# Kernel tuning notes

Hardware: AMD Instinct MI355X
Metric: run time of the kernel (lower is better)

## Reference

```python
import jax, jax.numpy as jnp
import numpy as np

NEG_SLOPE = 0.2  # PyG GATv2Conv default negative_slope


def gatv2_conv(x, src, dst, Wl, Wr, att, bias, concat):
    # x: [N, Fin]; src/dst: [E]; Wl/Wr: [Fin, H*C]; att: [H, C]
    N = x.shape[0]
    H, C = att.shape
    xl = (x @ Wl).reshape(N, H, C)
    xr = (x @ Wr).reshape(N, H, C)
    m = jax.nn.leaky_relu(xl[src] + xr[dst], NEG_SLOPE)          # [E,H,C]
    logits = jnp.einsum('ehc,hc->eh', m, att)                    # [E,H]
    lmax = jax.ops.segment_max(logits, dst, num_segments=N)      # stable softmax per dst segment
    ex = jnp.exp(logits - lmax[dst])
    denom = jax.ops.segment_sum(ex, dst, num_segments=N)
    alpha = ex / (denom[dst] + 1e-16)
    out = jax.ops.segment_sum(xl[src] * alpha[:, :, None], dst, num_segments=N)  # [N,H,C]
    out = out.reshape(N, H * C) if concat else out.mean(axis=1)
    return out + bias


def setup_inputs() -> dict:
    key = jax.random.key(0)
    ks = jax.random.split(key, 9)
    bsz, T, n_nodes = 8, 100, 2048
    Cin, hid, H, Cout = 128, 64, 4, 128
    inp = jax.random.normal(ks[0], (bsz, T, n_nodes), jnp.float32)
    ei = jax.random.randint(ks[1], (2, 32768), 0, n_nodes, jnp.int32)
    # remove self loops (PyG remove_self_loops before adding them back)
    ei = ei.at[1].set(jnp.where(ei[0] == ei[1], (ei[1] + 1) % n_nodes, ei[1]))

    def lin(k, fi, fo):
        return jax.random.normal(k, (fi, fo), jnp.float32) / np.sqrt(fi).astype(np.float32)

    return {
        'input': inp, 'edge_index': ei,
        'W_temb': lin(ks[2], T, Cin), 'b_temb': jnp.zeros((Cin,), jnp.float32),
        'Wl1': lin(ks[3], Cin, H * hid), 'Wr1': lin(ks[4], Cin, H * hid),
        'att1': jax.random.normal(ks[5], (H, hid), jnp.float32) / np.sqrt(hid).astype(np.float32),
        'b1': jnp.zeros((H * hid,), jnp.float32),
        'Wl2': lin(ks[6], H * hid, Cout), 'Wr2': lin(ks[7], H * hid, Cout),
        'att2': jax.random.normal(ks[8], (1, Cout), jnp.float32) / np.sqrt(Cout).astype(np.float32),
        'b2': jnp.zeros((Cout,), jnp.float32),
    }


def reference(input, edge_index, W_temb, b_temb, Wl1, Wr1, att1, b1, Wl2, Wr2, att2, b2):
    bsz, T, n_nodes = input.shape
    N = bsz * n_nodes
    # temporal embedding: [B,T,n] -> [B,n,T] @ [T,Cin] -> flatten to [N,Cin]
    x = (jnp.swapaxes(input, 1, 2) @ W_temb + b_temb).reshape(N, -1)
    # faithful to source: edge_index.repeat(1, bsz) tiles edges with NO batch offset;
    # GATv2Conv then adds self loops over all N nodes
    loops = jnp.arange(N, dtype=edge_index.dtype)
    src = jnp.concatenate([jnp.tile(edge_index[0], bsz), loops])
    dst = jnp.concatenate([jnp.tile(edge_index[1], bsz), loops])
    x = gatv2_conv(x, src, dst, Wl1, Wr1, att1, b1, True)
    x = jax.nn.elu(x)
    x = gatv2_conv(x, src, dst, Wl2, Wr2, att2, b2, False)
    return x.reshape(bsz, n_nodes, -1).mean(axis=1)  # [bsz, out_channels]
```

## Files before the change

kernel.cpp:

```cpp
#include <hip/hip_runtime.h>
#include <hip/hip_bf16.h>
#include <math.h>

#define NEG_SLOPE 0.2f

constexpr int BSZ = 8, T = 100, NN = 2048, N = BSZ * NN;
constexpr int CIN = 128, F1 = 256, F2 = 128;
constexpr int E = 32768;
constexpr int KP = 40;
constexpr int MAXDEG = 64;

typedef _Float16 f16x8 __attribute__((ext_vector_type(8)));
typedef float f32x4 __attribute__((ext_vector_type(4)));

__device__ inline float lrelu(float m) { return m > 0.f ? m : NEG_SLOPE * m; }
__device__ inline float eluf(float v) { return v > 0.f ? v : expm1f(v); }

__global__ __launch_bounds__(256) void k_prep(const float* __restrict__ Wt,
        const float* __restrict__ Wl1, const float* __restrict__ Wr1,
        const float* __restrict__ Wl2, const float* __restrict__ Wr2,
        const float* __restrict__ b2,
        _Float16* __restrict__ Tt, _Float16* __restrict__ T1l,
        _Float16* __restrict__ T1r, _Float16* __restrict__ T2l,
        _Float16* __restrict__ T2r, int* __restrict__ cnt, float* __restrict__ out) {
    __shared__ _Float16 tile[32][33];
    const int job = blockIdx.x;
    const int t = threadIdx.x;
    if (job == 144) {
        for (int i = t; i < NN; i += 256) cnt[i] = 0;
        for (int i = t; i < BSZ * F2; i += 256) out[i] = b2[i & (F2 - 1)];
        return;
    }
    int which, base;
    if (job < 16)       { which = 0; base = 0; }
    else if (job < 48)  { which = 1; base = 16; }
    else if (job < 80)  { which = 2; base = 48; }
    else if (job < 112) { which = 3; base = 80; }
    else                { which = 4; base = 112; }
    const int Ks[5] = {100, 128, 128, 256, 256};
    const int Kd[5] = {128, 128, 128, 256, 256};
    const int Nc[5] = {128, 256, 256, 128, 128};
    const float* Wsrc[5] = {Wt, Wl1, Wr1, Wl2, Wr2};
    _Float16* Wdst[5] = {Tt, T1l, T1r, T2l, T2r};
    int rel = job - base;
    int ks = Ks[which], kd = Kd[which], nc = Nc[which];
    int tilesN = nc / 32;
    int tk = (rel / tilesN) * 32, tn = (rel % tilesN) * 32;
    const float* src = Wsrc[which];
    _Float16* dst = Wdst[which];
    int tx = t & 31, ty = t >> 5;
    for (int r = ty; r < 32; r += 8)
        tile[r][tx] = (tk + r < ks) ? (_Float16)src[(tk + r) * nc + tn + tx] : (_Float16)0.f;
    __syncthreads();
    for (int r = ty; r < 32; r += 8)
        dst[(tn + r) * kd + tk + tx] = tile[tx][r];
}

__global__ __launch_bounds__(512) void k_gm1(const float* __restrict__ in,
        const _Float16* __restrict__ Tt, const float* __restrict__ bt,
        const _Float16* __restrict__ T1l, const _Float16* __restrict__ T1r,
        const float* __restrict__ b1, const _Float16* __restrict__ T2l,
        const int* __restrict__ ei, int* __restrict__ cnt, int* __restrict__ srcs,
        float* __restrict__ xl1, float* __restrict__ xr1,
        _Float16* __restrict__ h1h, float* __restrict__ out) {
    const int t = threadIdx.x;
    if (blockIdx.x >= 512) {
        int i = (blockIdx.x - 512) * 512 + t;
        int d = ei[E + i];
        int slot = atomicAdd(&cnt[d], 1);
        if (slot < MAXDEG) srcs[d * MAXDEG + slot] = ei[i];
        return;
    }
    __shared__ __align__(16) char smem[8704 + 43520];
    _Float16* xt = (_Float16*)smem;
    char* sh = smem + 8704;
    const int wave = t >> 6, lane = t & 63;
    const int quad = lane >> 4, l15 = lane & 15;
    const int mat = wave >> 2, cg4 = wave & 3;
    const int row0 = blockIdx.x * 32;
    _Float16* stgT = (_Float16*)sh;
    _Float16* inA  = (_Float16*)(sh + 34816);
    #pragma unroll
    for (int it = 0; it < 4; ++it) {
        int idx = t + it * 512;
        int col = idx >> 4, j = idx & 15;
        *(f16x8*)&stgT[col * 136 + j * 8] = *(const f16x8*)&Tt[col * 128 + j * 8];
    }
    {
        const int b = row0 >> 11, node0 = row0 & (NN - 1);
        const float* ip = in + (size_t)b * T * NN + node0;
        #pragma unroll
        for (int it = 0; it < 8; ++it) {
            int idx = t + it * 512;
            int tt = idx >> 5, n = idx & 31;
            inA[n * 136 + tt] = (tt < T) ? (_Float16)ip[tt * NN + n] : (_Float16)0.f;
        }
    }
    __syncthreads();
    {
        const int wcol = wave * 16 + l15;
        f32x4 a0 = {0,0,0,0}, a1 = {0,0,0,0};
        #pragma unroll
        for (int kt = 0; kt < 128; kt += 32) {
            f16x8 af0 = *(const f16x8*)&inA[l15 * 136 + kt + quad * 8];
            f16x8 af1 = *(const f16x8*)&inA[(16 + l15) * 136 + kt + quad * 8];
            f16x8 bf  = *(const f16x8*)&stgT[wcol * 136 + kt + quad * 8];
            a0 = __builtin_amdgcn_mfma_f32_16x16x32_f16(af0, bf, a0, 0, 0, 0);
            a1 = __builtin_amdgcn_mfma_f32_16x16x32_f16(af1, bf, a1, 0, 0, 0);
        }
        float bv = bt[wcol];
        #pragma unroll
        for (int r = 0; r < 4; ++r) {
            xt[(quad * 4 + r) * 136 + wcol]      = (_Float16)(a0[r] + bv);
            xt[(16 + quad * 4 + r) * 136 + wcol] = (_Float16)(a1[r] + bv);
        }
    }
    __syncthreads();
    _Float16* stg = (_Float16*)sh;
    const int nmats = (row0 < NN) ? 2 : 1;
    f32x4 acc[2][4];
    #pragma unroll
    for (int s = 0; s < 2; ++s)
        #pragma unroll
        for (int c = 0; c < 4; ++c) acc[s][c] = (f32x4){0,0,0,0};
    for (int kt = 0; kt < CIN; kt += 32) {
        if (kt) __syncthreads();
        for (int it = 0; it < nmats * 2; ++it) {
            int idx = t + it * 512;
            int m = idx >> 10, rem = idx & 1023;
            int col = rem >> 2, j = rem & 3;
            const _Float16* src = (m ? T1r : T1l) + col * CIN + kt + j * 8;
            *(f16x8*)&stg[(m * 256 + col) * KP + j * 8] = *(const f16x8*)src;
        }
        __syncthreads();
        f16x8 af0 = *(const f16x8*)&xt[l15 * 136 + kt + quad * 8];
        f16x8 af1 = *(const f16x8*)&xt[(16 + l15) * 136 + kt + quad * 8];
        if (mat < nmats) {
            #pragma unroll
            for (int ct = 0; ct < 4; ++ct) {
                int col = cg4 * 64 + ct * 16 + l15;
                f16x8 bf = *(const f16x8*)&stg[(mat * 256 + col) * KP + quad * 8];
                acc[0][ct] = __builtin_amdgcn_mfma_f32_16x16x32_f16(af0, bf, acc[0][ct], 0, 0, 0);
                acc[1][ct] = __builtin_amdgcn_mfma_f32_16x16x32_f16(af1, bf, acc[1][ct], 0, 0, 0);
            }
        }
    }
    if (row0 < NN) {
        float* dst = mat ? xr1 : xl1;
        #pragma unroll
        for (int s = 0; s < 2; ++s)
            #pragma unroll
            for (int ct = 0; ct < 4; ++ct) {
                int col = cg4 * 64 + ct * 16 + l15;
                #pragma unroll
                for (int r = 0; r < 4; ++r)
                    dst[(row0 + s * 16 + quad * 4 + r) * F1 + col] = acc[s][ct][r];
            }
        return;
    }
    __syncthreads();
    _Float16* stg2 = (_Float16*)sh;
    _Float16* hrow = (_Float16*)(sh + 10240);
    if (mat == 0) {
        #pragma unroll
        for (int ct = 0; ct < 4; ++ct) {
            int col = cg4 * 64 + ct * 16 + l15;
            float bv = b1[col];
            #pragma unroll
            for (int s = 0; s < 2; ++s)
                #pragma unroll
                for (int r = 0; r < 4; ++r)
                    hrow[(s * 16 + quad * 4 + r) * 264 + col] =
                        (_Float16)eluf(acc[s][ct][r] + bv);
        }
    }
    __syncthreads();
    f32x4 c0 = {0,0,0,0}, c1 = {0,0,0,0};
    const int colw = wave * 16 + l15;
    for (int kt = 0; kt < F1; kt += 32) {
        if (kt) __syncthreads();
        {
            int col = t >> 2, j = t & 3;
            *(f16x8*)&stg2[col * KP + j * 8] = *(const f16x8*)&T2l[col * F1 + kt + j * 8];
        }
        __syncthreads();
        f16x8 a0 = *(const f16x8*)&hrow[l15 * 264 + kt + quad * 8];
        f16x8 a1 = *(const f16x8*)&hrow[(16 + l15) * 264 + kt + quad * 8];
        f16x8 bf = *(const f16x8*)&stg2[colw * KP + quad * 8];
        c0 = __builtin_amdgcn_mfma_f32_16x16x32_f16(a0, bf, c0, 0, 0, 0);
        c1 = __builtin_amdgcn_mfma_f32_16x16x32_f16(a1, bf, c1, 0, 0, 0);
    }
    float s8 = c0[0] + c0[1] + c0[2] + c0[3] + c1[0] + c1[1] + c1[2] + c1[3];
    s8 += __shfl_xor(s8, 16, 64);
    s8 += __shfl_xor(s8, 32, 64);
    if (quad == 0)
        atomicAdd(&out[(row0 >> 11) * F2 + colw], s8 * (1.0f / NN));
}

__global__ __launch_bounds__(256) void k_gat1(const int* __restrict__ cnt,
        const int* __restrict__ srcs, const float* __restrict__ xl1,
        const float* __restrict__ xr1, const float* __restrict__ att1,
        const float* __restrict__ b1, _Float16* __restrict__ h1h) {
    __shared__ float lacc[4][F1];
    __shared__ float ldn[4][4];
    const int t = threadIdx.x;
    const int wv = t >> 6, c = t & 63;
    const int d = blockIdx.x;
    int deg = cnt[d]; deg = deg < MAXDEG ? deg : MAXDEG;
    float b[4], at[4], sh[4], acc[4] = {0,0,0,0}, dnl[4] = {0,0,0,0};
    #pragma unroll
    for (int k = 0; k < 4; ++k) {
        b[k]  = xr1[d * F1 + c + 64 * k];
        at[k] = att1[c + 64 * k];
        sh[k] = lrelu(xl1[d * F1 + c + 64 * k] + b[k]) * at[k];
    }
    #pragma unroll
    for (int o = 32; o; o >>= 1) {
        #pragma unroll
        for (int k = 0; k < 4; ++k) sh[k] += __shfl_xor(sh[k], o, 64);
    }
    for (int e = wv; e < deg; e += 4) {
        int s = srcs[d * MAXDEG + e];
        float a[4], p[4];
        #pragma unroll
        for (int k = 0; k < 4; ++k) {
            a[k] = xl1[s * F1 + c + 64 * k];
            p[k] = lrelu(a[k] + b[k]) * at[k];
        }
        #pragma unroll
        for (int o = 32; o; o >>= 1) {
            #pragma unroll
            for (int k = 0; k < 4; ++k) p[k] += __shfl_xor(p[k], o, 64);
        }
        #pragma unroll
        for (int k = 0; k < 4; ++k) {
            float w = 8.0f * __expf(p[k] - sh[k]);
            dnl[k] += w;
            acc[k] = fmaf(w, a[k], acc[k]);
        }
    }
    #pragma unroll
    for (int k = 0; k < 4; ++k) lacc[wv][c + 64 * k] = acc[k];
    if (c < 4) ldn[wv][c] = dnl[c];
    __syncthreads();
    int f = t, h = t >> 6;
    float tot = xl1[d * F1 + f] + lacc[0][f] + lacc[1][f] + lacc[2][f] + lacc[3][f];
    float dnf = 1.0f + ldn[0][h] + ldn[1][h] + ldn[2][h] + ldn[3][h];
    h1h[(size_t)d * F1 + f] = (_Float16)eluf(tot / (dnf + 1e-16f) + b1[f]);
}

__global__ __launch_bounds__(512) void k_gm2loc(const _Float16* __restrict__ h1h,
        const _Float16* __restrict__ T2l, const _Float16* __restrict__ T2r,
        float* __restrict__ xl2, float* __restrict__ xr2) {
    __shared__ __align__(16) _Float16 bs[2 * 128 * KP];
    const int t = threadIdx.x;
    const int wave = t >> 6, lane = t & 63;
    const int quad = lane >> 4, l15 = lane & 15;
    const int mat = wave >> 2, cg4 = wave & 3;
    const int row0 = blockIdx.x * 32;
    f32x4 acc[2][2];
    #pragma unroll
    for (int s = 0; s < 2; ++s)
        #pragma unroll
        for (int c = 0; c < 2; ++c) acc[s][c] = (f32x4){0,0,0,0};
    for (int kt = 0; kt < F1; kt += 32) {
        if (kt) __syncthreads();
        #pragma unroll
        for (int it = 0; it < 2; ++it) {
            int idx = t + it * 512;
            int m = idx >> 9, rem = idx & 511;
            int col = rem >> 2, j = rem & 3;
            const _Float16* src = (m ? T2r : T2l) + col * F1 + kt + j * 8;
            *(f16x8*)&bs[(m * 128 + col) * KP + j * 8] = *(const f16x8*)src;
        }
        __syncthreads();
        f16x8 af0 = *(const f16x8*)&h1h[(size_t)(row0 + l15) * F1 + kt + quad * 8];
        f16x8 af1 = *(const f16x8*)&h1h[(size_t)(row0 + 16 + l15) * F1 + kt + quad * 8];
        #pragma unroll
        for (int ct = 0; ct < 2; ++ct) {
            int col = cg4 * 32 + ct * 16 + l15;
            f16x8 bf = *(const f16x8*)&bs[(mat * 128 + col) * KP + quad * 8];
            acc[0][ct] = __builtin_amdgcn_mfma_f32_16x16x32_f16(af0, bf, acc[0][ct], 0, 0, 0);
            acc[1][ct] = __builtin_amdgcn_mfma_f32_16x16x32_f16(af1, bf, acc[1][ct], 0, 0, 0);
        }
    }
    float* dst = mat ? xr2 : xl2;
    #pragma unroll
    for (int s = 0; s < 2; ++s)
        #pragma unroll
        for (int ct = 0; ct < 2; ++ct) {
            int col = cg4 * 32 + ct * 16 + l15;
            #pragma unroll
            for (int r = 0; r < 4; ++r)
                dst[(row0 + s * 16 + quad * 4 + r) * F2 + col] = acc[s][ct][r];
        }
}

__global__ __launch_bounds__(256) void k_gat2(const int* __restrict__ cnt,
        const int* __restrict__ srcs, const float* __restrict__ xl2,
        const float* __restrict__ xr2, const float* __restrict__ att2,
        float* __restrict__ acc2) {
    const int d = blockIdx.x;
    const int t = threadIdx.x;
    const int wv = t >> 6, c = t & 63;
    int deg = cnt[d]; deg = deg < MAXDEG ? deg : MAXDEG;
    float b0 = xr2[d * F2 + c], b1v = xr2[d * F2 + c + 64];
    float at0 = att2[c], at1 = att2[c + 64];
    float sh = lrelu(xl2[d * F2 + c] + b0) * at0 + lrelu(xl2[d * F2 + c + 64] + b1v) * at1;
    #pragma unroll
    for (int o = 32; o; o >>= 1) sh += __shfl_xor(sh, o, 64);
    float acc0 = 0.f, acc1v = 0.f, dnl = 0.f;
    for (int e = wv; e < deg; e += 4) {
        int s = srcs[d * MAXDEG + e];
        float a0 = xl2[s * F2 + c], a1 = xl2[s * F2 + c + 64];
        float p = lrelu(a0 + b0) * at0 + lrelu(a1 + b1v) * at1;
        #pragma unroll
        for (int o = 32; o; o >>= 1) p += __shfl_xor(p, o, 64);
        float w = 8.0f * __expf(p - sh);
        dnl += w;
        acc0 = fmaf(w, a0, acc0);
        acc1v = fmaf(w, a1, acc1v);
    }
    __shared__ float lacc[4][F2];
    __shared__ float ldn[4];
    lacc[wv][c] = acc0;
    lacc[wv][c + 64] = acc1v;
    if (c == 0) ldn[wv] = dnl;
    __syncthreads();
    if (t < F2) {
        int f = t;
        float dnf = 1.0f + ldn[0] + ldn[1] + ldn[2] + ldn[3] + 1e-16f;
        acc2[d * F2 + f] =
            (xl2[d * F2 + f] + lacc[0][f] + lacc[1][f] + lacc[2][f] + lacc[3][f]) / dnf;
    }
}

__global__ __launch_bounds__(128) void k_out0(const float* __restrict__ acc2,
        float* __restrict__ out) {
    int chunk = blockIdx.x;
    int c = threadIdx.x;
    float s = 0.f;
    int n0 = chunk * 64;
    #pragma unroll 8
    for (int i = 0; i < 64; ++i)
        s += acc2[(n0 + i) * F2 + c];
    atomicAdd(&out[c], s * (1.0f / NN));
}

extern "C" void kernel_launch(void* const* d_in, const int* in_sizes, int n_in,
                              void* d_out, int out_size, void* d_ws, size_t ws_size,
                              hipStream_t stream) {
    const float* in   = (const float*)d_in[0];
    const int*   ei   = (const int*)d_in[1];
    const float* Wt   = (const float*)d_in[2];
    const float* bt   = (const float*)d_in[3];
    const float* Wl1  = (const float*)d_in[4];
    const float* Wr1  = (const float*)d_in[5];
    const float* att1 = (const float*)d_in[6];
    const float* b1   = (const float*)d_in[7];
    const float* Wl2  = (const float*)d_in[8];
    const float* Wr2  = (const float*)d_in[9];
    const float* att2 = (const float*)d_in[10];
    const float* b2   = (const float*)d_in[11];
    float* out = (float*)d_out;

    float* ws = (float*)d_ws;
    _Float16* h1h = (_Float16*)ws;
    float* xl1  = (float*)(h1h + (size_t)NN * F1);
    float* xr1  = xl1 + NN * F1;
    float* xl2  = xr1 + NN * F1;
    float* xr2  = xl2 + NN * F2;
    float* acc2 = xr2 + NN * F2;
    _Float16* Tt  = (_Float16*)(acc2 + NN * F2);
    _Float16* T1l = Tt + 128 * 128;
    _Float16* T1r = T1l + 256 * 128;
    _Float16* T2l = T1r + 256 * 128;
    _Float16* T2r = T2l + 128 * 256;
    int* cnt  = (int*)(T2r + 128 * 256);
    int* srcs = cnt + NN;

    k_prep<<<145, 256, 0, stream>>>(Wt, Wl1, Wr1, Wl2, Wr2, b2,
                                    Tt, T1l, T1r, T2l, T2r, cnt, out);
    k_gm1<<<576, 512, 0, stream>>>(in, Tt, bt, T1l, T1r, b1, T2l, ei, cnt, srcs,
                                   xl1, xr1, h1h, out);
    k_gat1<<<2048, 256, 0, stream>>>(cnt, srcs, xl1, xr1, att1, b1, h1h);
    k_gm2loc<<<64, 512, 0, stream>>>(h1h, T2l, T2r, xl2, xr2);
    k_gat2<<<NN, 256, 0, stream>>>(cnt, srcs, xl2, xr2, att2, acc2);
    k_out0<<<32, 128, 0, stream>>>(acc2, out);
}
```

Measured before the change: 134.2 us.

## Read GEMM weight fragments directly from global, unroll edge loops by two

The GEMM kernels stop staging transposed weight tiles through LDS and instead load MFMA B-fragments straight from global/L2. This removes the barriers and LDS traffic and cuts the shared-memory footprint of k_gm1. k_gm2loc is retiled to 16-row blocks with 256 threads, doubling its grid. Both GAT aggregation kernels now handle two edges per wave iteration so gather loads and shuffle reductions can overlap. The cost is uncoalesced, redundant global reads of the weights and higher register pressure.

After: 133.6 us. Within noise of the previous version (-0.4%).

```diff
diff --git a/kernel.cpp b/kernel.cpp
--- a/kernel.cpp
+++ b/kernel.cpp
@@ -7,7 +7,6 @@
 constexpr int BSZ = 8, T = 100, NN = 2048, N = BSZ * NN;
 constexpr int CIN = 128, F1 = 256, F2 = 128;
 constexpr int E = 32768;
-constexpr int KP = 40;
 constexpr int MAXDEG = 64;
 
 typedef _Float16 f16x8 __attribute__((ext_vector_type(8)));
@@ -61,8 +60,7 @@
         const _Float16* __restrict__ T1l, const _Float16* __restrict__ T1r,
         const float* __restrict__ b1, const _Float16* __restrict__ T2l,
         const int* __restrict__ ei, int* __restrict__ cnt, int* __restrict__ srcs,
-        float* __restrict__ xl1, float* __restrict__ xr1,
-        _Float16* __restrict__ h1h, float* __restrict__ out) {
+        float* __restrict__ xl1, float* __restrict__ xr1, float* __restrict__ out) {
     const int t = threadIdx.x;
     if (blockIdx.x >= 512) {
         int i = (blockIdx.x - 512) * 512 + t;
@@ -71,21 +69,13 @@
         if (slot < MAXDEG) srcs[d * MAXDEG + slot] = ei[i];
         return;
     }
-    __shared__ __align__(16) char smem[8704 + 43520];
-    _Float16* xt = (_Float16*)smem;
-    char* sh = smem + 8704;
+    __shared__ __align__(16) char smem[8704 + 16896];
+    _Float16* xt  = (_Float16*)smem;
+    _Float16* inA = (_Float16*)(smem + 8704);
     const int wave = t >> 6, lane = t & 63;
     const int quad = lane >> 4, l15 = lane & 15;
     const int mat = wave >> 2, cg4 = wave & 3;
     const int row0 = blockIdx.x * 32;
-    _Float16* stgT = (_Float16*)sh;
-    _Float16* inA  = (_Float16*)(sh + 34816);
-    #pragma unroll
-    for (int it = 0; it < 4; ++it) {
-        int idx = t + it * 512;
-        int col = idx >> 4, j = idx & 15;
-        *(f16x8*)&stgT[col * 136 + j * 8] = *(const f16x8*)&Tt[col * 128 + j * 8];
-    }
     {
         const int b = row0 >> 11, node0 = row0 & (NN - 1);
         const float* ip = in + (size_t)b * T * NN + node0;
@@ -104,7 +94,7 @@
         for (int kt = 0; kt < 128; kt += 32) {
             f16x8 af0 = *(const f16x8*)&inA[l15 * 136 + kt + quad * 8];
             f16x8 af1 = *(const f16x8*)&inA[(16 + l15) * 136 + kt + quad * 8];
-            f16x8 bf  = *(const f16x8*)&stgT[wcol * 136 + kt + quad * 8];
+            f16x8 bf  = *(const f16x8*)&Tt[wcol * 128 + kt + quad * 8];
             a0 = __builtin_amdgcn_mfma_f32_16x16x32_f16(af0, bf, a0, 0, 0, 0);
             a1 = __builtin_amdgcn_mfma_f32_16x16x32_f16(af1, bf, a1, 0, 0, 0);
         }
@@ -116,30 +106,22 @@
         }
     }
     __syncthreads();
-    _Float16* stg = (_Float16*)sh;
     const int nmats = (row0 < NN) ? 2 : 1;
     f32x4 acc[2][4];
     #pragma unroll
     for (int s = 0; s < 2; ++s)
         #pragma unroll
         for (int c = 0; c < 4; ++c) acc[s][c] = (f32x4){0,0,0,0};
-    for (int kt = 0; kt < CIN; kt += 32) {
-        if (kt) __syncthreads();
-        for (int it = 0; it < nmats * 2; ++it) {
-            int idx = t + it * 512;
-            int m = idx >> 10, rem = idx & 1023;
-            int col = rem >> 2, j = rem & 3;
-            const _Float16* src = (m ? T1r : T1l) + col * CIN + kt + j * 8;
-            *(f16x8*)&stg[(m * 256 + col) * KP + j * 8] = *(const f16x8*)src;
-        }
-        __syncthreads();
-        f16x8 af0 = *(const f16x8*)&xt[l15 * 136 + kt + quad * 8];
-        f16x8 af1 = *(const f16x8*)&xt[(16 + l15) * 136 + kt + quad * 8];
-        if (mat < nmats) {
+    if (mat < nmats) {
+        const _Float16* Tm = mat ? T1r : T1l;
+        #pragma unroll
+        for (int kt = 0; kt < CIN; kt += 32) {
+            f16x8 af0 = *(const f16x8*)&xt[l15 * 136 + kt + quad * 8];
+            f16x8 af1 = *(const f16x8*)&xt[(16 + l15) * 136 + kt + quad * 8];
             #pragma unroll
             for (int ct = 0; ct < 4; ++ct) {
                 int col = cg4 * 64 + ct * 16 + l15;
-                f16x8 bf = *(const f16x8*)&stg[(mat * 256 + col) * KP + quad * 8];
+                f16x8 bf = *(const f16x8*)&Tm[col * CIN + kt + quad * 8];
                 acc[0][ct] = __builtin_amdgcn_mfma_f32_16x16x32_f16(af0, bf, acc[0][ct], 0, 0, 0);
                 acc[1][ct] = __builtin_amdgcn_mfma_f32_16x16x32_f16(af1, bf, acc[1][ct], 0, 0, 0);
             }
@@ -158,9 +140,7 @@
             }
         return;
     }
-    __syncthreads();
-    _Float16* stg2 = (_Float16*)sh;
-    _Float16* hrow = (_Float16*)(sh + 10240);
+    _Float16* hrow = (_Float16*)(smem + 8704);
     if (mat == 0) {
         #pragma unroll
         for (int ct = 0; ct < 4; ++ct) {
@@ -177,16 +157,11 @@
     __syncthreads();
     f32x4 c0 = {0,0,0,0}, c1 = {0,0,0,0};
     const int colw = wave * 16 + l15;
+    #pragma unroll
     for (int kt = 0; kt < F1; kt += 32) {
-        if (kt) __syncthreads();
-        {
-            int col = t >> 2, j = t & 3;
-            *(f16x8*)&stg2[col * KP + j * 8] = *(const f16x8*)&T2l[col * F1 + kt + j * 8];
-        }
-        __syncthreads();
         f16x8 a0 = *(const f16x8*)&hrow[l15 * 264 + kt + quad * 8];
         f16x8 a1 = *(const f16x8*)&hrow[(16 + l15) * 264 + kt + quad * 8];
-        f16x8 bf = *(const f16x8*)&stg2[colw * KP + quad * 8];
+        f16x8 bf = *(const f16x8*)&T2l[colw * F1 + kt + quad * 8];
         c0 = __builtin_amdgcn_mfma_f32_16x16x32_f16(a0, bf, c0, 0, 0, 0);
         c1 = __builtin_amdgcn_mfma_f32_16x16x32_f16(a1, bf, c1, 0, 0, 0);
     }
@@ -219,24 +194,35 @@
         #pragma unroll
         for (int k = 0; k < 4; ++k) sh[k] += __shfl_xor(sh[k], o, 64);
     }
-    for (int e = wv; e < deg; e += 4) {
-        int s = srcs[d * MAXDEG + e];
-        float a[4], p[4];
+    for (int e = wv; e < deg; e += 8) {
+        bool v2 = (e + 4) < deg;
+        int s  = srcs[d * MAXDEG + e];
+        int s2 = v2 ? srcs[d * MAXDEG + e + 4] : s;
+        float a[4], p[4], a2[4], p2[4];
         #pragma unroll
         for (int k = 0; k < 4; ++k) {
-            a[k] = xl1[s * F1 + c + 64 * k];
-            p[k] = lrelu(a[k] + b[k]) * at[k];
+            a[k]  = xl1[s  * F1 + c + 64 * k];
+            a2[k] = xl1[s2 * F1 + c + 64 * k];
+        }
+        #pragma unroll
+        for (int k = 0; k < 4; ++k) {
+            p[k]  = lrelu(a[k]  + b[k]) * at[k];
+            p2[k] = lrelu(a2[k] + b[k]) * at[k];
         }
         #pragma unroll
         for (int o = 32; o; o >>= 1) {
             #pragma unroll
-            for (int k = 0; k < 4; ++k) p[k] += __shfl_xor(p[k], o, 64);
+            for (int k = 0; k < 4; ++k) {
+                p[k]  += __shfl_xor(p[k],  o, 64);
+                p2[k] += __shfl_xor(p2[k], o, 64);
+            }
         }
         #pragma unroll
         for (int k = 0; k < 4; ++k) {
-            float w = 8.0f * __expf(p[k] - sh[k]);
-            dnl[k] += w;
-            acc[k] = fmaf(w, a[k], acc[k]);
+            float w  = 8.0f * __expf(p[k] - sh[k]);
+            float w2 = v2 ? 8.0f * __expf(p2[k] - sh[k]) : 0.f;
+            dnl[k] += w + w2;
+            acc[k] = fmaf(w, a[k], fmaf(w2, a2[k], acc[k]));
         }
     }
     #pragma unroll
@@ -249,51 +235,36 @@
     h1h[(size_t)d * F1 + f] = (_Float16)eluf(tot / (dnf + 1e-16f) + b1[f]);
 }
 
-__global__ __launch_bounds__(512) void k_gm2loc(const _Float16* __restrict__ h1h,
+__global__ __launch_bounds__(256) void k_gm2loc(const _Float16* __restrict__ h1h,
         const _Float16* __restrict__ T2l, const _Float16* __restrict__ T2r,
         float* __restrict__ xl2, float* __restrict__ xr2) {
-    __shared__ __align__(16) _Float16 bs[2 * 128 * KP];
     const int t = threadIdx.x;
     const int wave = t >> 6, lane = t & 63;
     const int quad = lane >> 4, l15 = lane & 15;
-    const int mat = wave >> 2, cg4 = wave & 3;
-    const int row0 = blockIdx.x * 32;
-    f32x4 acc[2][2];
-    #pragma unroll
-    for (int s = 0; s < 2; ++s)
-        #pragma unroll
-        for (int c = 0; c < 2; ++c) acc[s][c] = (f32x4){0,0,0,0};
+    const int mat = wave >> 1, cg = wave & 1;
+    const int row0 = blockIdx.x * 16;
+    const _Float16* Tm = mat ? T2r : T2l;
+    f32x4 acc[4];
+    #pragma unroll
+    for (int c = 0; c < 4; ++c) acc[c] = (f32x4){0,0,0,0};
+    #pragma unroll
     for (int kt = 0; kt < F1; kt += 32) {
-        if (kt) __syncthreads();
-        #pragma unroll
-        for (int it = 0; it < 2; ++it) {
-            int idx = t + it * 512;
-            int m = idx >> 9, rem = idx & 511;
-            int col = rem >> 2, j = rem & 3;
-            const _Float16* src = (m ? T2r : T2l) + col * F1 + kt + j * 8;
-            *(f16x8*)&bs[(m * 128 + col) * KP + j * 8] = *(const f16x8*)src;
-        }
-        __syncthreads();
-        f16x8 af0 = *(const f16x8*)&h1h[(size_t)(row0 + l15) * F1 + kt + quad * 8];
-        f16x8 af1 = *(const f16x8*)&h1h[(size_t)(row0 + 16 + l15) * F1 + kt + quad * 8];
-        #pragma unroll
-        for (int ct = 0; ct < 2; ++ct) {
-            int col = cg4 * 32 + ct * 16 + l15;
-            f16x8 bf = *(const f16x8*)&bs[(mat * 128 + col) * KP + quad * 8];
-            acc[0][ct] = __builtin_amdgcn_mfma_f32_16x16x32_f16(af0, bf, acc[0][ct], 0, 0, 0);
-            acc[1][ct] = __builtin_amdgcn_mfma_f32_16x16x32_f16(af1, bf, acc[1][ct], 0, 0, 0);
+        f16x8 af = *(const f16x8*)&h1h[(size_t)(row0 + l15) * F1 + kt + quad * 8];
+        #pragma unroll
+        for (int ct = 0; ct < 4; ++ct) {
+            int col = cg * 64 + ct * 16 + l15;
+            f16x8 bf = *(const f16x8*)&Tm[col * F1 + kt + quad * 8];
+            acc[ct] = __builtin_amdgcn_mfma_f32_16x16x32_f16(af, bf, acc[ct], 0, 0, 0);
         }
     }
     float* dst = mat ? xr2 : xl2;
     #pragma unroll
-    for (int s = 0; s < 2; ++s)
-        #pragma unroll
-        for (int ct = 0; ct < 2; ++ct) {
-            int col = cg4 * 32 + ct * 16 + l15;
-            #pragma unroll
-            for (int r = 0; r < 4; ++r)
-                dst[(row0 + s * 16 + quad * 4 + r) * F2 + col] = acc[s][ct][r];
-        }
+    for (int ct = 0; ct < 4; ++ct) {
+        int col = cg * 64 + ct * 16 + l15;
+        #pragma unroll
+        for (int r = 0; r < 4; ++r)
+            dst[(row0 + quad * 4 + r) * F2 + col] = acc[ct][r];
+    }
 }
 
 __global__ __launch_bounds__(256) void k_gat2(const int* __restrict__ cnt,
@@ -310,16 +281,24 @@
     #pragma unroll
     for (int o = 32; o; o >>= 1) sh += __shfl_xor(sh, o, 64);
     float acc0 = 0.f, acc1v = 0.f, dnl = 0.f;
-    for (int e = wv; e < deg; e += 4) {
-        int s = srcs[d * MAXDEG + e];
-        float a0 = xl2[s * F2 + c], a1 = xl2[s * F2 + c + 64];
+    for (int e = wv; e < deg; e += 8) {
+        bool v2 = (e + 4) < deg;
+        int s  = srcs[d * MAXDEG + e];
+        int s2 = v2 ? srcs[d * MAXDEG + e + 4] : s;
+        float a0 = xl2[s  * F2 + c], a1 = xl2[s  * F2 + c + 64];
+        float e0 = xl2[s2 * F2 + c], e1 = xl2[s2 * F2 + c + 64];
         float p = lrelu(a0 + b0) * at0 + lrelu(a1 + b1v) * at1;
-        #pragma unroll
-        for (int o = 32; o; o >>= 1) p += __shfl_xor(p, o, 64);
-        float w = 8.0f * __expf(p - sh);
-        dnl += w;
-        acc0 = fmaf(w, a0, acc0);
-        acc1v = fmaf(w, a1, acc1v);
+        float q = lrelu(e0 + b0) * at0 + lrelu(e1 + b1v) * at1;
+        #pragma unroll
+        for (int o = 32; o; o >>= 1) {
+            p += __shfl_xor(p, o, 64);
+            q += __shfl_xor(q, o, 64);
+        }
+        float w  = 8.0f * __expf(p - sh);
+        float w2 = v2 ? 8.0f * __expf(q - sh) : 0.f;
+        dnl += w + w2;
+        acc0  = fmaf(w, a0, fmaf(w2, e0, acc0));
+        acc1v = fmaf(w, a1, fmaf(w2, e1, acc1v));
     }
     __shared__ float lacc[4][F2];
     __shared__ float ldn[4];
@@ -382,9 +361,9 @@
     k_prep<<<145, 256, 0, stream>>>(Wt, Wl1, Wr1, Wl2, Wr2, b2,
                                     Tt, T1l, T1r, T2l, T2r, cnt, out);
     k_gm1<<<576, 512, 0, stream>>>(in, Tt, bt, T1l, T1r, b1, T2l, ei, cnt, srcs,
-                                   xl1, xr1, h1h, out);
+                                   xl1, xr1, out);
     k_gat1<<<2048, 256, 0, stream>>>(cnt, srcs, xl1, xr1, att1, b1, h1h);
-    k_gm2loc<<<64, 512, 0, stream>>>(h1h, T2l, T2r, xl2, xr2);
+    k_gm2loc<<<128, 256, 0, stream>>>(h1h, T2l, T2r, xl2, xr2);
     k_gat2<<<NN, 256, 0, stream>>>(cnt, srcs, xl2, xr2, att2, acc2);
     k_out0<<<32, 128, 0, stream>>>(acc2, out);
 }
```
